# Kernel tuning notes

Hardware: AMD Instinct MI355X
Metric: run time of the kernel (lower is better)

Reference implementation:

```python
import jax, jax.numpy as jnp
import numpy as np

N_ENTITIES = 200000
DIM = 512  # even: split into real/imag halves of 256


def setup_inputs() -> dict:
    key = jax.random.key(0)
    k1, k2, k3 = jax.random.split(key, 3)
    return {
        "head_entity": jax.random.normal(k1, (DIM,), dtype=jnp.float32),
        "question_embedding": jax.random.normal(k2, (DIM,), dtype=jnp.float32),
        "entity_embeddings": jax.random.normal(k3, (N_ENTITIES, DIM), dtype=jnp.float32),
    }


def _complex_scores(head_entity, question_embedding, entity_embeddings):
    # ComplEx scoring: split each embedding into real/imag halves,
    # rotate head by question in the complex plane, dot with all entities.
    h_re, h_im = jnp.split(head_entity, 2)            # [d/2] each
    q_re, q_im = jnp.split(question_embedding, 2)     # [d/2]
    e_re, e_im = jnp.split(entity_embeddings, 2, axis=1)  # [N, d/2]
    s_re = h_re * q_re - h_im * q_im                  # [d/2]
    s_im = h_re * q_im + h_im * q_re                  # [d/2]
    # scores[n] = <s_re, e_re[n]> + <s_im, e_im[n]>  (single fused GEMV)
    return e_re @ s_re + e_im @ s_im                  # [N]


def reference(head_entity, question_embedding, entity_embeddings):
    scores = _complex_scores(head_entity, question_embedding, entity_embeddings)
    best_entity_idx = jnp.argmax(scores)
    return entity_embeddings[best_entity_idx]         # [DIM]
```

## Files before the change

kernel.cpp:

```cpp
#include <hip/hip_runtime.h>


#define N_ENT 200000
#define DIM 512
#define HALF 256

#define BLOCKS 2048
#define TPB 256
#define WAVES_PER_BLOCK (TPB / 64)
#define TOTAL_WAVES (BLOCKS * WAVES_PER_BLOCK)

__global__ __launch_bounds__(TPB) void complex_score_kernel(
    const float* __restrict__ head,
    const float* __restrict__ quest,
    const float* __restrict__ ents,
    float* __restrict__ blk_score,
    int* __restrict__ blk_idx)
{
    __shared__ float s[DIM];

    const int t = threadIdx.x;

    if (t < HALF) {
        const float hre = head[t],  him = head[t + HALF];
        const float qre = quest[t], qim = quest[t + HALF];
        s[t]        = hre * qre - him * qim;
        s[t + HALF] = hre * qim + him * qre;
    }
    __syncthreads();

    const int lane  = t & 63;
    const int wid   = t >> 6;
    const int gwave = blockIdx.x * WAVES_PER_BLOCK + wid;

    const float4 s0 = *(const float4*)(&s[lane * 4]);
    const float4 s1 = *(const float4*)(&s[HALF + lane * 4]);

    float best = -1e30f;
    int   bidx = 0x7fffffff;

    for (int row = gwave; row < N_ENT; row += TOTAL_WAVES) {
        const float4* p = (const float4*)(ents + (size_t)row * DIM);
        const float4 a = p[lane];
        const float4 b = p[64 + lane];

        float acc = a.x * s0.x + a.y * s0.y + a.z * s0.z + a.w * s0.w
                  + b.x * s1.x + b.y * s1.y + b.z * s1.z + b.w * s1.w;

        #pragma unroll
        for (int off = 32; off > 0; off >>= 1)
            acc += __shfl_xor(acc, off, 64);

        if (acc > best) { best = acc; bidx = row; }
    }

    __shared__ float wscore[WAVES_PER_BLOCK];
    __shared__ int   widx[WAVES_PER_BLOCK];
    if (lane == 0) { wscore[wid] = best; widx[wid] = bidx; }
    __syncthreads();

    if (t == 0) {
        float bs = wscore[0];
        int   bi = widx[0];
        #pragma unroll
        for (int i = 1; i < WAVES_PER_BLOCK; ++i) {
            if (wscore[i] > bs || (wscore[i] == bs && widx[i] < bi)) {
                bs = wscore[i];
                bi = widx[i];
            }
        }
        blk_score[blockIdx.x] = bs;
        blk_idx[blockIdx.x]   = bi;
    }
}

__global__ __launch_bounds__(256) void argmax_gather_kernel(
    const float* __restrict__ blk_score,
    const int* __restrict__ blk_idx,
    const float* __restrict__ ents,
    float* __restrict__ out)
{
    __shared__ float ss[256];
    __shared__ int   si[256];

    const int t = threadIdx.x;
    float bs = -1e30f;
    int   bi = 0x7fffffff;

    for (int i = t; i < BLOCKS; i += 256) {
        const float v  = blk_score[i];
        const int   ix = blk_idx[i];
        if (v > bs || (v == bs && ix < bi)) { bs = v; bi = ix; }
    }
    ss[t] = bs;
    si[t] = bi;
    __syncthreads();

    for (int stride = 128; stride > 0; stride >>= 1) {
        if (t < stride) {
            if (ss[t + stride] > ss[t] ||
                (ss[t + stride] == ss[t] && si[t + stride] < si[t])) {
                ss[t] = ss[t + stride];
                si[t] = si[t + stride];
            }
        }
        __syncthreads();
    }

    const int best = si[0];
    if (t < 128) {
        ((float4*)out)[t] = ((const float4*)(ents + (size_t)best * DIM))[t];
    }
}

extern "C" void kernel_launch(void* const* d_in, const int* in_sizes, int n_in,
                              void* d_out, int out_size, void* d_ws, size_t ws_size,
                              hipStream_t stream) {
    const float* head  = (const float*)d_in[0];
    const float* quest = (const float*)d_in[1];
    const float* ents  = (const float*)d_in[2];
    float* out = (float*)d_out;

    float* blk_score = (float*)d_ws;
    int*   blk_idx   = (int*)((char*)d_ws + BLOCKS * sizeof(float));

    complex_score_kernel<<<BLOCKS, TPB, 0, stream>>>(head, quest, ents,
                                                     blk_score, blk_idx);
    argmax_gather_kernel<<<1, 256, 0, stream>>>(blk_score, blk_idx, ents, out);
}
```

Measured before the change: 537.1 us.

## Process four rows per wave with transpose-style shuffle reduction

Each wave now loads four consecutive entity rows per iteration, giving more independent loads in flight. The four dot products are reduced with a butterfly that exchanges partial sums, so the reduction costs about half as many shuffles per row as four separate reductions. Each lane group tracks the best of one row slot, and a final cross-lane argmax reduction runs before the block reduction. It uses more registers per thread, and because N is divisible by four there is no tail handling.

```diff
diff --git a/kernel.cpp b/kernel.cpp
--- a/kernel.cpp
+++ b/kernel.cpp
@@ -7,8 +7,10 @@
 
 #define BLOCKS 2048
 #define TPB 256
-#define WAVES_PER_BLOCK (TPB / 64)
-#define TOTAL_WAVES (BLOCKS * WAVES_PER_BLOCK)
+#define WPB (TPB / 64)
+#define TOTAL_WAVES (BLOCKS * WPB)
+#define ROWS_PER_ITER 4
+#define SWEEP (TOTAL_WAVES * ROWS_PER_ITER)
 
 __global__ __launch_bounds__(TPB) void complex_score_kernel(
     const float* __restrict__ head,
@@ -31,31 +33,58 @@
 
     const int lane  = t & 63;
     const int wid   = t >> 6;
-    const int gwave = blockIdx.x * WAVES_PER_BLOCK + wid;
+    const int gwave = blockIdx.x * WPB + wid;
 
     const float4 s0 = *(const float4*)(&s[lane * 4]);
     const float4 s1 = *(const float4*)(&s[HALF + lane * 4]);
 
-    float best = -1e30f;
+    float best = -3.4e38f;
     int   bidx = 0x7fffffff;
 
-    for (int row = gwave; row < N_ENT; row += TOTAL_WAVES) {
-        const float4* p = (const float4*)(ents + (size_t)row * DIM);
-        const float4 a = p[lane];
-        const float4 b = p[64 + lane];
+    for (int base = gwave * ROWS_PER_ITER; base < N_ENT; base += SWEEP) {
+        const float4* p = (const float4*)(ents + (size_t)base * DIM);
 
-        float acc = a.x * s0.x + a.y * s0.y + a.z * s0.z + a.w * s0.w
-                  + b.x * s1.x + b.y * s1.y + b.z * s1.z + b.w * s1.w;
+        const float4 a0 = p[lane],       b0 = p[64 + lane];
+        const float4 a1 = p[128 + lane], b1 = p[192 + lane];
+        const float4 a2 = p[256 + lane], b2 = p[320 + lane];
+        const float4 a3 = p[384 + lane], b3 = p[448 + lane];
 
-        #pragma unroll
-        for (int off = 32; off > 0; off >>= 1)
-            acc += __shfl_xor(acc, off, 64);
+        float acc0 = a0.x*s0.x + a0.y*s0.y + a0.z*s0.z + a0.w*s0.w
+                   + b0.x*s1.x + b0.y*s1.y + b0.z*s1.z + b0.w*s1.w;
+        float acc1 = a1.x*s0.x + a1.y*s0.y + a1.z*s0.z + a1.w*s0.w
+                   + b1.x*s1.x + b1.y*s1.y + b1.z*s1.z + b1.w*s1.w;
+        float acc2 = a2.x*s0.x + a2.y*s0.y + a2.z*s0.z + a2.w*s0.w
+                   + b2.x*s1.x + b2.y*s1.y + b2.z*s1.z + b2.w*s1.w;
+        float acc3 = a3.x*s0.x + a3.y*s0.y + a3.z*s0.z + a3.w*s0.w
+                   + b3.x*s1.x + b3.y*s1.y + b3.z*s1.z + b3.w*s1.w;
 
-        if (acc > best) { best = acc; bidx = row; }
+        const float x0 = acc0 + __shfl_xor(acc0, 1, 64);
+        const float x1 = acc1 + __shfl_xor(acc1, 1, 64);
+        const float x2 = acc2 + __shfl_xor(acc2, 1, 64);
+        const float x3 = acc3 + __shfl_xor(acc3, 1, 64);
+        const float c01 = (lane & 1) ? x1 : x0;
+        const float c23 = (lane & 1) ? x3 : x2;
+        const float y01 = c01 + __shfl_xor(c01, 2, 64);
+        const float y23 = c23 + __shfl_xor(c23, 2, 64);
+        float r = (lane & 2) ? y23 : y01;
+        r += __shfl_xor(r, 4, 64);
+        r += __shfl_xor(r, 8, 64);
+        r += __shfl_xor(r, 16, 64);
+        r += __shfl_xor(r, 32, 64);
+
+        const int row = base + (lane & 3);
+        if (r > best) { best = r; bidx = row; }
     }
 
-    __shared__ float wscore[WAVES_PER_BLOCK];
-    __shared__ int   widx[WAVES_PER_BLOCK];
+    #pragma unroll
+    for (int off = 32; off > 0; off >>= 1) {
+        const float ob = __shfl_xor(best, off, 64);
+        const int   oi = __shfl_xor(bidx, off, 64);
+        if (ob > best || (ob == best && oi < bidx)) { best = ob; bidx = oi; }
+    }
+
+    __shared__ float wscore[WPB];
+    __shared__ int   widx[WPB];
     if (lane == 0) { wscore[wid] = best; widx[wid] = bidx; }
     __syncthreads();
 
@@ -63,7 +92,7 @@
         float bs = wscore[0];
         int   bi = widx[0];
         #pragma unroll
-        for (int i = 1; i < WAVES_PER_BLOCK; ++i) {
+        for (int i = 1; i < WPB; ++i) {
             if (wscore[i] > bs || (wscore[i] == bs && widx[i] < bi)) {
                 bs = wscore[i];
                 bi = widx[i];
@@ -84,7 +113,7 @@
     __shared__ int   si[256];
 
     const int t = threadIdx.x;
-    float bs = -1e30f;
+    float bs = -3.4e38f;
     int   bi = 0x7fffffff;
 
     for (int i = t; i < BLOCKS; i += 256) {
```

New measurement: 534.8 us. No clear change (-0.4%).
